# Kernel tuning notes

Measured on AMD Instinct MI355X. Metric: run time of the kernel, lower is better.

The kernel has to match this reference:

```python
import jax, jax.numpy as jnp
import numpy as np

G, K1, K2, N, NP, EPS = 16, 128, 32, 128, 512, 1e-5

def _bn(x, axes):
    m = jnp.mean(x, axes, keepdims=True)
    v = jnp.var(x, axes, keepdims=True)  # biased, as torch BN training mode
    return (x - m) * jax.lax.rsqrt(v + EPS)

def _fps(xyz, npoint):
    # farthest point sampling, deterministic start at index 0; xyz (B,P,3)
    B, P, _ = xyz.shape
    def step(carry, _):
        dists, far = carry
        c = jnp.take_along_axis(xyz, far[:, None, None], axis=1)   # (B,1,3)
        d = jnp.sum((xyz - c) ** 2, -1)                            # (B,P)
        dists = jnp.minimum(dists, d)
        return (dists, jnp.argmax(dists, -1)), far
    init = (jnp.full((B, P), 1e10, xyz.dtype), jnp.zeros((B,), jnp.int32))
    _, idx = jax.lax.scan(step, init, None, length=npoint)         # (npoint,B)
    return jnp.take_along_axis(xyz, idx.T[:, :, None], axis=1)     # (B,npoint,3)

def _pointnet(x, w1, b1, w2, b2, w3, b3):
    h = jax.nn.relu(_bn(x @ w1 + b1, (0, 1)))
    h = jax.nn.relu(_bn(h @ w2 + b2, (0, 1)))
    h = _bn(h @ w3 + b3, (0, 1))
    return jnp.max(h, axis=1)                                      # (B,1024)

def _mapping(feat, w1, b1, w2, b2, w3, b3, w4, b4):
    # all 16 branches stacked on leading axis g
    h = jax.nn.relu(_bn(jnp.einsum('bk,gkj->gbj', feat, w1) + b1[:, None, :], (1,)))
    h = jax.nn.relu(_bn(jnp.einsum('gbj,gjk->gbk', h, w2) + b2[:, None, :], (1,)))
    h = jax.nn.relu(_bn(jnp.einsum('gbj,gjk->gbk', h, w3) + b3[:, None, :], (1,)))
    return jax.nn.relu(_bn(jnp.einsum('gbj,gjk->gbk', h, w4) + b4[:, None, :], (1,)))

def _axform(feat, fw, fb, c1w, c1b, c2w, c2b, c3w, c3b, c4w, c4b):
    # feat (G,B,K1); 1x1 convs expressed as einsums in channels-last layout
    xb = (jnp.einsum('gbk,gkm->gbm', feat, fw) + fb[:, None, :]).reshape(G, -1, N, K2)
    h = jax.nn.relu(_bn(jnp.einsum('gbnk,gkc->gbnc', xb, c1w) + c1b[:, None, None, :], (1, 2)))
    h = jax.nn.relu(_bn(jnp.einsum('gbnc,gcd->gbnd', h, c2w) + c2b[:, None, None, :], (1, 2)))
    h = jnp.einsum('gbnd,gde->gbne', h, c3w) + c3b[:, None, None, :]  # (G,B,N,1024)
    w = jax.nn.softmax(h, axis=2)                                     # softmax over N
    y = jnp.einsum('gbne,gbnk->gbek', w, xb)                          # (G,B,1024,K2)
    return jnp.einsum('gbek,gkc->gbec', y, c4w) + c4b[:, None, None, :]  # (G,B,1024,3)

def _forward(x, pn, mp, gen, ref):
    x_partial = _fps(x, NP)                                           # (B,512,3)
    feat = _pointnet(x, *pn)                                          # (B,1024)
    mfeat = _mapping(feat, *mp)                                       # (G,B,K1)
    x1g = _axform(mfeat, *gen)                                        # (G,B,1024,3)
    B = x.shape[0]
    x_1 = jnp.transpose(x1g, (1, 0, 2, 3)).reshape(B, -1, 3)          # (B,16384,3)
    fps1 = jax.vmap(lambda p: _fps(p, NP))(x1g)                       # (G,B,512,3)
    x_base = jnp.concatenate([fps1, jnp.broadcast_to(x_partial, (G,) + x_partial.shape)], axis=2)
    x2g = x_base + _axform(mfeat, *ref)                               # (G,B,1024,3)
    x_2 = jnp.transpose(x2g, (1, 0, 2, 3)).reshape(B, -1, 3)
    return x_1, x_2

def setup_inputs() -> dict:
    keys = iter(jax.random.split(jax.random.key(0), 40))
    def rn(shape, s=0.02):
        return (s * jax.random.normal(next(keys), shape)).astype(jnp.float32)
    inp = {}
    inp['x'] = jax.random.normal(next(keys), (16, 2048, 3), jnp.float32)
    inp['pn_w1'] = rn((3, 64));      inp['pn_b1'] = rn((64,))
    inp['pn_w2'] = rn((64, 128));    inp['pn_b2'] = rn((128,))
    inp['pn_w3'] = rn((128, 1024));  inp['pn_b3'] = rn((1024,))
    inp['mp_w1'] = rn((G, 1024, 1024)); inp['mp_b1'] = rn((G, 1024))
    inp['mp_w2'] = rn((G, 1024, 1024)); inp['mp_b2'] = rn((G, 1024))
    inp['mp_w3'] = rn((G, 1024, 1024)); inp['mp_b3'] = rn((G, 1024))
    inp['mp_w4'] = rn((G, 1024, K1));   inp['mp_b4'] = rn((G, K1))
    for p in ('g', 'r'):
        inp[p + '_fw'] = rn((G, K1, N * K2)); inp[p + '_fb'] = rn((G, N * K2))
        inp[p + '_c1w'] = rn((G, K2, 64));    inp[p + '_c1b'] = rn((G, 64))
        inp[p + '_c2w'] = rn((G, 64, 128));   inp[p + '_c2b'] = rn((G, 128))
        inp[p + '_c3w'] = rn((G, 128, 1024)); inp[p + '_c3b'] = rn((G, 1024))
        inp[p + '_c4w'] = rn((G, K2, 3));     inp[p + '_c4b'] = rn((G, 3))
    return inp

def reference(x, pn_w1, pn_b1, pn_w2, pn_b2, pn_w3, pn_b3,
              mp_w1, mp_b1, mp_w2, mp_b2, mp_w3, mp_b3, mp_w4, mp_b4,
              g_fw, g_fb, g_c1w, g_c1b, g_c2w, g_c2b, g_c3w, g_c3b, g_c4w, g_c4b,
              r_fw, r_fb, r_c1w, r_c1b, r_c2w, r_c2b, r_c3w, r_c3b, r_c4w, r_c4b):
    pn = (pn_w1, pn_b1, pn_w2, pn_b2, pn_w3, pn_b3)
    mp = (mp_w1, mp_b1, mp_w2, mp_b2, mp_w3, mp_b3, mp_w4, mp_b4)
    gen = (g_fw, g_fb, g_c1w, g_c1b, g_c2w, g_c2b, g_c3w, g_c3b, g_c4w, g_c4b)
    ref = (r_fw, r_fb, r_c1w, r_c1b, r_c2w, r_c2b, r_c3w, r_c3b, r_c4w, r_c4b)
    return _forward(x, pn, mp, gen, ref)
```

## Files before the change

### kernel.cpp

```cpp
#include <hip/hip_runtime.h>
#include <math.h>

#define TID ((int)threadIdx.x)

namespace {
constexpr float EPSf = 1e-5f;

typedef __attribute__((ext_vector_type(8))) short short8;
typedef __attribute__((ext_vector_type(4))) float f32x4;

struct FpsArgs {
  const float* pts; float* out; float* dmin; int* far;
  int it0, it1, nc;
};

__device__ __forceinline__ unsigned fenc(float f){
  unsigned u = __float_as_uint(f);
  return (u & 0x80000000u) ? ~u : (u | 0x80000000u);
}
__device__ __forceinline__ float fdec(unsigned e){
  unsigned u = (e & 0x80000000u) ? (e & 0x7fffffffu) : ~e;
  return __uint_as_float(u);
}
__device__ __forceinline__ short bf16rne(float f){
  unsigned u = __float_as_uint(f);
  return (short)((u + 0x7fffu + ((u >> 16) & 1u)) >> 16);
}

template<int CTRL>
__device__ __forceinline__ void dpp_comb(float& bm, int& bp){
  int om_i = __builtin_amdgcn_update_dpp(__float_as_int(bm), __float_as_int(bm), CTRL, 0xf, 0xf, false);
  int op   = __builtin_amdgcn_update_dpp(bp, bp, CTRL, 0xf, 0xf, false);
  float om = __int_as_float(om_i);
  if (om > bm || (om == bm && op < bp)){ bm = om; bp = op; }
}

template<int LP, int NT>
__device__ void fps_body(const FpsArgs& a, int ci){
  const int NPTS = NT*LP;
  const float* pts = a.pts + (size_t)ci * NPTS * 3;
  float* out = a.out + (size_t)ci * 512 * 3;
  float* dst = a.dmin + (size_t)ci * NPTS;
  float px[LP], py[LP], pz[LP], dmin[LP];
#pragma unroll
  for (int j = 0; j < LP; j++){
    int p = TID + NT*j;
    px[j] = pts[p*3+0]; py[j] = pts[p*3+1]; pz[j] = pts[p*3+2];
  }
  int far;
  if (a.it0 == 0){
#pragma unroll
    for (int j = 0; j < LP; j++) dmin[j] = 1e10f;
    far = 0;
  } else {
#pragma unroll
    for (int j = 0; j < LP; j++) dmin[j] = dst[TID + NT*j];
    far = a.far[ci];
  }
  __shared__ unsigned long long red2[2][NT/64];
  for (int i = a.it0; i < a.it1; i++){
    float cx = pts[far*3+0], cy = pts[far*3+1], cz = pts[far*3+2];
    if (TID == 0){ out[i*3+0]=cx; out[i*3+1]=cy; out[i*3+2]=cz; }
    float bm = -1.f; int bp = 0;
#pragma unroll
    for (int j = 0; j < LP; j++){
      float dx = __fsub_rn(px[j], cx);
      float dy = __fsub_rn(py[j], cy);
      float dz = __fsub_rn(pz[j], cz);
      float d  = __fadd_rn(__fadd_rn(__fmul_rn(dx,dx), __fmul_rn(dy,dy)), __fmul_rn(dz,dz));
      float dm = fminf(dmin[j], d);
      dmin[j] = dm;
      if (dm > bm){ bm = dm; bp = TID + NT*j; }
    }
    dpp_comb<0x111>(bm,bp); dpp_comb<0x112>(bm,bp); dpp_comb<0x114>(bm,bp);
    dpp_comb<0x118>(bm,bp); dpp_comb<0x142>(bm,bp); dpp_comb<0x143>(bm,bp);
    unsigned long long key =
      ((unsigned long long)(unsigned)__builtin_amdgcn_readlane(__float_as_int(bm), 63) << 32)
      | (unsigned)~(unsigned)__builtin_amdgcn_readlane(bp, 63);
    if ((TID & 63) == 63) red2[i&1][TID>>6] = key;
    __syncthreads();
    unsigned long long kk = red2[i&1][0];
#pragma unroll
    for (int t = 1; t < NT/64; t++){
      unsigned long long o = red2[i&1][t];
      kk = kk > o ? kk : o;
    }
    far = (int)~(unsigned)kk;
  }
  if (a.it1 < 512){
#pragma unroll
    for (int j = 0; j < LP; j++) dst[TID + NT*j] = dmin[j];
    if (TID == 0) a.far[ci] = far;
  }
}

template<int C, int K, int FLP>
__global__ void __launch_bounds__(256) rowgemm_kernel(const float* __restrict__ in,
    const float* __restrict__ w, const float* __restrict__ bias, const float2* __restrict__ st2,
    float* __restrict__ out, int rows_per_g, FpsArgs fa)
{
  int bid = blockIdx.x;
  if constexpr (FLP > 0){
    if (bid < fa.nc){ fps_body<FLP,256>(fa, bid); return; }
    bid -= fa.nc;
  }
  constexpr int RPB = 256 / C;
  __shared__ float lin[RPB * K];
  size_t row0 = (size_t)bid * RPB;
  int g = (int)(row0 / rows_per_g);
  for (int i = TID; i < RPB*K; i += 256){
    float v = in[row0*(size_t)K + i];
    if (st2){ float2 s = st2[(size_t)g*K + (i % K)]; v = fmaxf((v - s.x)*s.y, 0.f); }
    lin[i] = v;
  }
  __syncthreads();
  int r = TID / C, c = TID % C;
  float acc = bias[(size_t)g*C + c];
  const float* wg = w + (size_t)g*K*C + c;
#pragma unroll
  for (int k = 0; k < K; k++) acc = fmaf(lin[r*K + k], wg[(size_t)k*C], acc);
  out[(row0 + r)*C + c] = acc;
}

template<int FLP>
__global__ void __launch_bounds__(256, 4) big1024m_kernel(const float* __restrict__ in,
    const float2* __restrict__ st2, const short* __restrict__ wtp,
    float* __restrict__ ps, float* __restrict__ pq, unsigned* __restrict__ maxenc, FpsArgs fa)
{
  int bid = blockIdx.x;
  if constexpr (FLP > 0){
    if (bid < fa.nc){ fps_body<FLP,256>(fa, bid); return; }
    bid -= fa.nc;
  }
  size_t row0 = (size_t)bid * 128;
  int b = (int)(row0 >> 11);
  __shared__ float2 sb[128];
  __shared__ float mS[512], mQ[512], mM[512];
  if (TID < 128) sb[TID] = st2[TID];
  __syncthreads();
  int lane = TID & 63, wid = TID >> 6, lr = lane & 15, lkg = lane >> 4;

  short8 afr[4][2];
  const float* src = in + row0*128;
#pragma unroll
  for (int kt = 0; kt < 4; kt++){
    int kb = kt*32 + lkg*8;
    float2 ss[8];
#pragma unroll
    for (int j = 0; j < 8; j++) ss[j] = sb[kb + j];
#pragma unroll
    for (int nt = 0; nt < 2; nt++){
      int row = wid*32 + nt*16 + lr;
      float4 a0 = *(const float4*)(src + row*128 + kb);
      float4 a1 = *(const float4*)(src + row*128 + kb + 4);
      const float vals[8] = {a0.x,a0.y,a0.z,a0.w,a1.x,a1.y,a1.z,a1.w};
      short8 ob;
#pragma unroll
      for (int j = 0; j < 8; j++)
        ob[j] = bf16rne(fmaxf((vals[j] - ss[j].x)*ss[j].y, 0.f));
      afr[kt][nt] = ob;
    }
  }

  for (int cs = 0; cs < 8; cs++){
    f32x4 acc[2][8];
#pragma unroll
    for (int nt = 0; nt < 2; nt++)
#pragma unroll
      for (int et = 0; et < 8; et++) acc[nt][et] = (f32x4){0.f,0.f,0.f,0.f};
    const short* wp = wtp + (size_t)(cs*128)*128;
#pragma unroll
    for (int kt = 0; kt < 4; kt++){
      int kb = kt*32 + lkg*8;
#pragma unroll
      for (int et = 0; et < 8; et++){
        short8 bfr = *(const short8*)&wp[(et*16 + lr)*128 + kb];
        acc[0][et] = __builtin_amdgcn_mfma_f32_16x16x32_bf16(afr[kt][0], bfr, acc[0][et], 0, 0, 0);
        acc[1][et] = __builtin_amdgcn_mfma_f32_16x16x32_bf16(afr[kt][1], bfr, acc[1][et], 0, 0, 0);
      }
    }
#pragma unroll
    for (int et = 0; et < 8; et++){
      float s = 0.f, q = 0.f, m = -1e38f;
#pragma unroll
      for (int nt = 0; nt < 2; nt++)
#pragma unroll
        for (int r = 0; r < 4; r++){
          float v = acc[nt][et][r];
          s += v; q = fmaf(v, v, q); m = fmaxf(m, v);
        }
      s += __shfl_xor(s, 16); s += __shfl_xor(s, 32);
      q += __shfl_xor(q, 16); q += __shfl_xor(q, 32);
      m = fmaxf(m, __shfl_xor(m, 16)); m = fmaxf(m, __shfl_xor(m, 32));
      if (lkg == 0){
        mS[wid*128 + et*16 + lr] = s;
        mQ[wid*128 + et*16 + lr] = q;
        mM[wid*128 + et*16 + lr] = m;
      }
    }
    __syncthreads();
    if (wid == 0){
#pragma unroll
      for (int t = 0; t < 2; t++){
        int c = t*64 + lane;
        float s4 = mS[c] + mS[128 + c] + mS[256 + c] + mS[384 + c];
        float q4 = mQ[c] + mQ[128 + c] + mQ[256 + c] + mQ[384 + c];
        float m4 = fmaxf(fmaxf(mM[c], mM[128 + c]), fmaxf(mM[256 + c], mM[384 + c]));
        ps[(size_t)bid*1024 + cs*128 + c] = s4;
        pq[(size_t)bid*1024 + cs*128 + c] = q4;
        atomicMax(&maxenc[(size_t)b*1024 + cs*128 + c], fenc(m4));
      }
    }
    __syncthreads();
  }
}

template<int FLP>
__global__ void __launch_bounds__(128) mapgemm2_kernel(const float* __restrict__ in, int in_gstride,
    const float* __restrict__ w, const float* __restrict__ bias, const float2* __restrict__ st2,
    float* __restrict__ out, int K, int J, int JB, int NS, FpsArgs fa)
{
  int bid = blockIdx.x;
  if constexpr (FLP > 0){
    if (bid < fa.nc){ fps_body<FLP,128>(fa, bid); return; }
    bid -= fa.nc;
  }
  int kc = bid / (JB*16);
  int g  = (bid / JB) % 16;
  int jb = bid % JB;
  int kchunk = K / NS, k0 = kc*kchunk;
  __shared__ float linT[128*16];
  const float* ing = in + (size_t)g * in_gstride;
  for (int i = TID; i < kchunk*16; i += 128){
    int b = i / kchunk, k = i - b*kchunk;
    float v = ing[(size_t)b*K + k0 + k];
    if (st2){ float2 s = st2[(size_t)g*K + k0 + k]; v = fmaxf((v - s.x)*s.y, 0.f); }
    linT[k*16 + b] = v;
  }
  __syncthreads();
  int bh = TID >> 6, jq = TID & 63;
  int j = jb*256 + jq*4;
  const float* wp = w + ((size_t)g*K + k0)*J + j;
  float4 a4[8];
#pragma unroll
  for (int bi = 0; bi < 8; bi++) a4[bi] = make_float4(0.f,0.f,0.f,0.f);
#pragma unroll 4
  for (int k = 0; k < kchunk; k++){
    float4 wv = *(const float4*)(wp + (size_t)k*J);
    float4 l0 = *(const float4*)&linT[k*16 + bh*8];
    float4 l1 = *(const float4*)&linT[k*16 + bh*8 + 4];
    const float lv[8] = {l0.x,l0.y,l0.z,l0.w,l1.x,l1.y,l1.z,l1.w};
#pragma unroll
    for (int bi = 0; bi < 8; bi++){
      a4[bi].x = fmaf(lv[bi], wv.x, a4[bi].x);
      a4[bi].y = fmaf(lv[bi], wv.y, a4[bi].y);
      a4[bi].z = fmaf(lv[bi], wv.z, a4[bi].z);
      a4[bi].w = fmaf(lv[bi], wv.w, a4[bi].w);
    }
  }
  if (NS == 1){
    float4 bv = *(const float4*)(bias + (size_t)g*J + j);
#pragma unroll
    for (int bi = 0; bi < 8; bi++){
      int b = bh*8 + bi;
      float4 o = make_float4(a4[bi].x+bv.x, a4[bi].y+bv.y, a4[bi].z+bv.z, a4[bi].w+bv.w);
      *(float4*)&out[((size_t)g*16 + b)*J + j] = o;
    }
  } else {
#pragma unroll
    for (int bi = 0; bi < 8; bi++)
      *(float4*)&out[(((size_t)kc*16 + g)*16 + bh*8 + bi)*J + j] = a4[bi];
  }
}

__global__ void __launch_bounds__(256) mapgemm_kernel(const float* __restrict__ in, int in_gstride,
    const float* __restrict__ w, const float* __restrict__ bias, const float2* __restrict__ st2,
    float* __restrict__ out, int K, int J, int JB, int NS)
{
  int bid = blockIdx.x;
  int kc = bid / (JB*16);
  int g  = (bid / JB) % 16;
  int jb = bid % JB;
  int j  = jb*256 + TID;
  bool jv = j < J;
  int jc = jv ? j : 0;
  int kchunk = K / NS;
  int k0 = kc * kchunk;
  __shared__ float lin[16 * 128];
  const float* ing = in + (size_t)g * in_gstride;
  float acc[16];
  float bv = (NS == 1 && jv) ? bias[(size_t)g*J + jc] : 0.f;
#pragma unroll
  for (int b = 0; b < 16; b++) acc[b] = bv;
  for (int kt = k0; kt < k0 + kchunk; kt += 128){
    __syncthreads();
    for (int i = TID; i < 2048; i += 256){
      int b = i >> 7, k = i & 127;
      float v = ing[(size_t)b*K + kt + k];
      if (st2){ float2 s = st2[(size_t)g*K + kt + k]; v = fmaxf((v - s.x)*s.y, 0.f); }
      lin[i] = v;
    }
    __syncthreads();
    const float* wg = w + ((size_t)g*K + kt)*J + jc;
    for (int k = 0; k < 128; k++){
      float wv = wg[(size_t)k*J];
#pragma unroll
      for (int b = 0; b < 16; b++) acc[b] = fmaf(lin[b*128 + k], wv, acc[b]);
    }
  }
  if (jv){
    if (NS == 1){
      for (int b = 0; b < 16; b++) out[((size_t)g*16 + b)*J + j] = acc[b];
    } else {
      for (int b = 0; b < 16; b++) out[(((size_t)kc*16 + g)*16 + b)*J + j] = acc[b];
    }
  }
}

__global__ void __launch_bounds__(256) redstats_kernel(const float* __restrict__ part,
    const float* __restrict__ bias, float* __restrict__ out, float2* __restrict__ st2,
    int J, int NS)
{
  int t = blockIdx.x*256 + TID;
  int g = t / J, j = t % J;
  float bv = bias[t];
  float s = 0.f, q = 0.f;
  for (int b = 0; b < 16; b++){
    float v = bv;
    for (int c = 0; c < NS; c++) v += part[(((size_t)c*16 + g)*16 + b)*J + j];
    out[((size_t)g*16 + b)*J + j] = v;
    s += v; q = fmaf(v, v, q);
  }
  float mean = s * (1.f/16.f);
  float var  = q * (1.f/16.f) - mean*mean;
  st2[t] = make_float2(mean, rsqrtf(fmaxf(var, 0.f) + EPSf));
}

template<int FLP>
__global__ void __launch_bounds__(256) statsacc_kernel(const float* __restrict__ in,
    float* __restrict__ part, int C, size_t chunk, FpsArgs fa)
{
  int bid = blockIdx.x;
  if constexpr (FLP > 0){
    if (bid < fa.nc){ fps_body<FLP,256>(fa, bid); return; }
    bid -= fa.nc;
  }
  size_t base = (size_t)bid * chunk;
  int c = TID % C;
  float s = 0.f, q = 0.f;
  for (size_t idx = base + TID; idx < base + chunk; idx += 256){
    float v = in[idx]; s += v; q = fmaf(v, v, q);
  }
  __shared__ float ls[256], lq[256];
  ls[TID] = s; lq[TID] = q; __syncthreads();
  if (TID < C){
    for (int t = TID + C; t < 256; t += C){ s += ls[t]; q += lq[t]; }
    part[((size_t)bid*C + c)*2]   = s;
    part[((size_t)bid*C + c)*2+1] = q;
  }
}

__global__ void statsfin_kernel(const float* __restrict__ part, float2* __restrict__ st2,
    int C, int G, float invR)
{
  int slot = blockIdx.x*256 + TID;
  if (slot >= G*C) return;
  int g = slot / C, c = slot % C;
  int bpg = 256 / G;
  float s = 0.f, q = 0.f;
  for (int b = 0; b < bpg; b++){
    size_t p = ((size_t)(g*bpg + b)*C + c)*2;
    s += part[p]; q += part[p+1];
  }
  float mean = s*invR;
  float var  = q*invR - mean*mean;
  st2[slot] = make_float2(mean, rsqrtf(fmaxf(var, 0.f) + EPSf));
}

__global__ void pnfin_kernel(const float* __restrict__ ps, const float* __restrict__ pq,
                             float2* __restrict__ st)
{
  int c = blockIdx.x*256 + TID;
  float s = 0.f, q = 0.f;
  for (int rb = 0; rb < 256; rb++){ s += ps[rb*1024 + c]; q += pq[rb*1024 + c]; }
  float mean = s * (1.f/32768.f);
  float var  = q * (1.f/32768.f) - mean*mean;
  st[c] = make_float2(mean, rsqrtf(fmaxf(var, 0.f) + EPSf));
}

__global__ void feat_kernel(const unsigned* __restrict__ me, const float2* __restrict__ st,
                            float* __restrict__ feat)
{
  int t = blockIdx.x*256 + TID;
  int c = t & 1023;
  float2 s = st[c];
  feat[t] = (fdec(me[t]) - s.x) * s.y;
}

__global__ void __launch_bounds__(256) wtr_kernel(const float* __restrict__ c3w,
                                                  short* __restrict__ wt)
{
  int g = blockIdx.x >> 4, kt = blockIdx.x & 15;
  __shared__ float lds[8*1024];
  const float* src = c3w + ((size_t)g*128 + kt*8)*1024;
  for (int i = TID; i < 8192; i += 256) lds[i] = src[i];
  __syncthreads();
  for (int e = TID; e < 1024; e += 256){
    short8 v;
#pragma unroll
    for (int j = 0; j < 8; j++) v[j] = bf16rne(lds[j*1024 + e]);
    *(short8*)&wt[((size_t)g*1024 + e)*128 + kt*8] = v;
  }
}

template<int FLP>
__global__ void __launch_bounds__(256, 2) fused_kernel(const float* __restrict__ c2o,
    const float2* __restrict__ st2, const short* __restrict__ wt,
    const float* __restrict__ xb, const float* __restrict__ c4w, const float* __restrict__ c4b,
    float* __restrict__ out_pts, float* __restrict__ out_x1, FpsArgs fa)
{
  int bid = blockIdx.x;
  if constexpr (FLP > 0){
    if (bid < fa.nc){ fps_body<FLP,256>(fa, bid); return; }
    bid -= fa.nc;
  }
  int gb = bid >> 1, ebh = bid & 1;
  int g = gb >> 4, b = gb & 15;
  __shared__ short Pbf[16384];
  __shared__ short Bls[16384];
  __shared__ short xbT[4096];
  __shared__ float2 sb[128];
  __shared__ float mred[512];

  if (TID < 128) sb[TID] = st2[(size_t)g*128 + TID];
  {
    const float* xsrc = xb + (size_t)gb*4096;
    for (int idx = TID; idx < 1024; idx += 256){
      int n = idx >> 3, k4 = (idx & 7)*4;
      float4 v = *(const float4*)(xsrc + n*32 + k4);
      const float vv[4] = {v.x, v.y, v.z, v.w};
#pragma unroll
      for (int j = 0; j < 4; j++){
        int k = k4 + j;
        xbT[k*128 + (((n >> 3) ^ (k & 7)) << 3) + (n & 7)] = bf16rne(vv[j]);
      }
    }
  }
  const int eb0 = ebh*4;
  const short* wt_base = wt + (size_t)g*1024*128;
  {
    const short* wtg = wt_base + (size_t)(eb0*128)*128;
    for (int i = TID; i < 2048; i += 256){
      int e = i >> 4, kc = i & 15;
      short8 v = *(const short8*)&wtg[e*128 + kc*8];
      *(short8*)&Bls[e*128 + ((kc ^ (e & 7)) << 3)] = v;
    }
  }

  int lane = TID & 63, wid = TID >> 6;
  int lr = lane & 15, lkg = lane >> 4;

  __syncthreads();

  short8 afr[4][2];
  const float* src = c2o + (size_t)gb*16384;
#pragma unroll
  for (int kt = 0; kt < 4; kt++){
    int kb = kt*32 + lkg*8;
    float2 ss[8];
#pragma unroll
    for (int j = 0; j < 8; j++) ss[j] = sb[kb + j];
#pragma unroll
    for (int nt = 0; nt < 2; nt++){
      int row = wid*32 + nt*16 + lr;
      float4 a0 = *(const float4*)(src + row*128 + kb);
      float4 a1 = *(const float4*)(src + row*128 + kb + 4);
      const float vals[8] = {a0.x,a0.y,a0.z,a0.w,a1.x,a1.y,a1.z,a1.w};
      short8 ob;
#pragma unroll
      for (int j = 0; j < 8; j++)
        ob[j] = bf16rne(fmaxf((vals[j] - ss[j].x)*ss[j].y, 0.f));
      afr[kt][nt] = ob;
    }
  }

  float c4l[2][3];
  {
    const float* cw = c4w + g*96;
#pragma unroll
    for (int kt2 = 0; kt2 < 2; kt2++){
      int k = kt2*16 + lr;
      c4l[kt2][0] = cw[k*3+0]; c4l[kt2][1] = cw[k*3+1]; c4l[kt2][2] = cw[k*3+2];
    }
  }
  float cb0 = c4b[g*3+0], cb1 = c4b[g*3+1], cb2 = c4b[g*3+2];
  unsigned* Pu = (unsigned*)Pbf;

  for (int eb = eb0; eb < eb0 + 4; eb++){
    f32x4 acc[2][8];
#pragma unroll
    for (int nt = 0; nt < 2; nt++)
#pragma unroll
      for (int et = 0; et < 8; et++) acc[nt][et] = (f32x4){0.f,0.f,0.f,0.f};
#pragma unroll
    for (int kt = 0; kt < 4; kt++){
      int kcf = kt*4 + lkg;
#pragma unroll
      for (int et = 0; et < 8; et++){
        int e = et*16 + lr;
        short8 bfr = *(const short8*)&Bls[e*128 + ((kcf ^ (e & 7)) << 3)];
        acc[0][et] = __builtin_amdgcn_mfma_f32_16x16x32_bf16(afr[kt][0], bfr, acc[0][et], 0, 0, 0);
        acc[1][et] = __builtin_amdgcn_mfma_f32_16x16x32_bf16(afr[kt][1], bfr, acc[1][et], 0, 0, 0);
      }
    }

    short8 bpre[8];
    bool havepre = (eb + 1 < eb0 + 4);
    if (havepre){
      const short* wtg = wt_base + (size_t)((eb+1)*128)*128;
#pragma unroll
      for (int ii = 0; ii < 8; ii++){
        int i = TID + 256*ii;
        int e = i >> 4, kc = i & 15;
        bpre[ii] = *(const short8*)&wtg[e*128 + kc*8];
      }
    }

#pragma unroll
    for (int et = 0; et < 8; et++){
      float ss = 0.f;
#pragma unroll
      for (int nt = 0; nt < 2; nt++)
#pragma unroll
        for (int r = 0; r < 4; r++){
          float p = __expf(acc[nt][et][r]);
          acc[nt][et][r] = p;
          ss += p;
        }
      ss += __shfl_xor(ss, 16);
      ss += __shfl_xor(ss, 32);
      if (lkg == 0) mred[wid*128 + et*16 + lr] = ss;
      int e = et*16 + lr;
#pragma unroll
      for (int nt = 0; nt < 2; nt++){
        int nb = wid*32 + nt*16 + lkg*4;
        int base = e*128 + ((((nb >> 3)) ^ (e & 7)) << 3) + (nb & 7);
        unsigned lo = (unsigned)(unsigned short)bf16rne(acc[nt][et][0])
                    | ((unsigned)(unsigned short)bf16rne(acc[nt][et][1]) << 16);
        unsigned hi = (unsigned)(unsigned short)bf16rne(acc[nt][et][2])
                    | ((unsigned)(unsigned short)bf16rne(acc[nt][et][3]) << 16);
        Pu[base >> 1]       = lo;
        Pu[(base >> 1) + 1] = hi;
      }
    }
    __syncthreads();

    if (havepre){
#pragma unroll
      for (int ii = 0; ii < 8; ii++){
        int i = TID + 256*ii;
        int e = i >> 4, kc = i & 15;
        *(short8*)&Bls[e*128 + ((kc ^ (e & 7)) << 3)] = bpre[ii];
      }
    }

    f32x4 yy[2][2];
#pragma unroll
    for (int t2 = 0; t2 < 2; t2++){ yy[t2][0] = (f32x4){0.f,0.f,0.f,0.f}; yy[t2][1] = (f32x4){0.f,0.f,0.f,0.f}; }
#pragma unroll
    for (int nc = 0; nc < 4; nc++){
      short8 bfrs[2];
#pragma unroll
      for (int kt2 = 0; kt2 < 2; kt2++){
        int k = kt2*16 + lr;
        bfrs[kt2] = *(const short8*)&xbT[k*128 + (((nc*4 + lkg) ^ (k & 7)) << 3)];
      }
#pragma unroll
      for (int t2 = 0; t2 < 2; t2++){
        int e = (wid*2 + t2)*16 + lr;
        short8 afrp = *(const short8*)&Pbf[e*128 + (((nc*4 + lkg) ^ (e & 7)) << 3)];
        yy[t2][0] = __builtin_amdgcn_mfma_f32_16x16x32_bf16(afrp, bfrs[0], yy[t2][0], 0, 0, 0);
        yy[t2][1] = __builtin_amdgcn_mfma_f32_16x16x32_bf16(afrp, bfrs[1], yy[t2][1], 0, 0, 0);
      }
    }

#pragma unroll
    for (int t2 = 0; t2 < 2; t2++){
#pragma unroll
      for (int r = 0; r < 4; r++){
        float o0 = yy[t2][0][r]*c4l[0][0] + yy[t2][1][r]*c4l[1][0];
        float o1 = yy[t2][0][r]*c4l[0][1] + yy[t2][1][r]*c4l[1][1];
        float o2 = yy[t2][0][r]*c4l[0][2] + yy[t2][1][r]*c4l[1][2];
#pragma unroll
        for (int d = 1; d < 16; d <<= 1){
          o0 += __shfl_xor(o0, d);
          o1 += __shfl_xor(o1, d);
          o2 += __shfl_xor(o2, d);
        }
        if (lr == 0){
          int e = (wid*2 + t2)*16 + lkg*4 + r;
          float s = mred[e] + mred[128 + e] + mred[256 + e] + mred[384 + e];
          float rs = 1.f / s;
          o0 = fmaf(o0, rs, cb0);
          o1 = fmaf(o1, rs, cb1);
          o2 = fmaf(o2, rs, cb2);
          int eg = eb*128 + e;
          size_t po = ((size_t)gb*1024 + eg)*3;
          out_pts[po+0] = o0; out_pts[po+1] = o1; out_pts[po+2] = o2;
          if (out_x1){
            size_t xo = (((size_t)b*16 + g)*1024 + eg)*3;
            out_x1[xo+0] = o0; out_x1[xo+1] = o1; out_x1[xo+2] = o2;
          }
        }
      }
    }
    __syncthreads();
  }
}

__global__ void combine_kernel(const float* __restrict__ fps1, const float* __restrict__ xpart,
                               const float* __restrict__ d2, float* __restrict__ x2)
{
  size_t i = (size_t)blockIdx.x*256 + TID;
  if (i >= (size_t)16*16*1024*3) return;
  int c = (int)(i % 3);
  size_t t = i / 3;
  int e = (int)(t % 1024);
  size_t gb = t / 1024;
  int g = (int)(gb >> 4), b = (int)(gb & 15);
  float base;
  if (e < 512) base = fps1[(gb*512 + e)*3 + c];
  else         base = xpart[((size_t)b*512 + (e - 512))*3 + c];
  x2[(((size_t)b*16384) + (size_t)g*1024 + e)*3 + c] = base + d2[i];
}

}

extern "C" void kernel_launch(void* const* d_in, const int* in_sizes, int n_in,
                              void* d_out, int out_size, void* d_ws, size_t ws_size,
                              hipStream_t stream)
{
  (void)in_sizes; (void)n_in; (void)out_size; (void)ws_size;
  const float* x    = (const float*)d_in[0];
  const float* pnw1 = (const float*)d_in[1];
  const float* pnb1 = (const float*)d_in[2];
  const float* pnw2 = (const float*)d_in[3];
  const float* pnb2 = (const float*)d_in[4];
  const float* pnw3 = (const float*)d_in[5];
  const float* mpw[4] = {(const float*)d_in[7],(const float*)d_in[9],(const float*)d_in[11],(const float*)d_in[13]};
  const float* mpb[4] = {(const float*)d_in[8],(const float*)d_in[10],(const float*)d_in[12],(const float*)d_in[14]};

  float* ws = (float*)d_ws;
  size_t o = 0;
  auto alloc = [&](size_t n){ float* p = ws + o; o += n; return p; };
  float* x_partial = alloc(24576);
  float* feat      = alloc(16384);
  float* mfeat     = alloc(32768);
  float2* st_pn1   = (float2*)alloc(128);
  float2* st_pn2   = (float2*)alloc(256);
  float2* st_pn3   = (float2*)alloc(2048);
  float2* st_c1    = (float2*)alloc(2048);
  float2* st_c2    = (float2*)alloc(4096);
  float2* st_map0  = (float2*)alloc(32768);
  float2* st_map1  = (float2*)alloc(32768);
  float2* st_map2  = (float2*)alloc(32768);
  float2* st_map3  = (float2*)alloc(4096);
  float* sa_part   = alloc(65536);
  float* pn_ps     = alloc(262144);
  float* pn_pq     = alloc(262144);
  unsigned* maxenc = (unsigned*)alloc(16384);
  float* mapA      = alloc(262144);
  float* mapB      = alloc(262144);
  float* mpart     = alloc(4194304);
  float* xb        = alloc(1048576);
  float* c1o       = alloc(2097152);
  float* c2o       = alloc(4194304);
  float* x1g       = alloc(786432);
  float* d2buf     = alloc(786432);
  float* fps1b     = alloc(393216);
  float* fpsA_dmin = alloc(32768);
  int*   fpsA_far  = (int*)alloc(16);
  float* fpsB_dmin = alloc(262144);
  int*   fpsB_far  = (int*)alloc(256);
  short* wt_g      = (short*)alloc(1048576);
  short* wt_r      = (short*)alloc(1048576);
  short* wt_pn     = (short*)alloc(65536);

  float* xout1 = (float*)d_out;
  float* xout2 = xout1 + 786432;

  hipMemsetAsync(maxenc, 0, 16384*sizeof(unsigned), stream);

  wtr_kernel<<<256, 256, 0, stream>>>((const float*)d_in[21], wt_g);
  wtr_kernel<<<256, 256, 0, stream>>>((const float*)d_in[31], wt_r);
  wtr_kernel<<<16, 256, 0, stream>>>(pnw3, wt_pn);

  FpsArgs f0{};
  FpsArgs fa{x, x_partial, fpsA_dmin, fpsA_far, 0, 0, 16};

  fa.it0 = 0; fa.it1 = 64;
  rowgemm_kernel<64,3,8><<<8192+16, 256, 0, stream>>>(x, pnw1, pnb1, nullptr, c1o, 32768, fa);
  statsacc_kernel<0><<<256, 256, 0, stream>>>(c1o, sa_part, 64, 8192, f0);
  statsfin_kernel<<<1, 256, 0, stream>>>(sa_part, st_pn1, 64, 1, 1.f/32768.f);
  fa.it0 = 64; fa.it1 = 128;
  rowgemm_kernel<128,64,8><<<16384+16, 256, 0, stream>>>(c1o, pnw2, pnb2, st_pn1, c2o, 32768, fa);
  statsacc_kernel<0><<<256, 256, 0, stream>>>(c2o, sa_part, 128, 16384, f0);
  statsfin_kernel<<<1, 256, 0, stream>>>(sa_part, st_pn2, 128, 1, 1.f/32768.f);
  fa.it0 = 128; fa.it1 = 224;
  big1024m_kernel<8><<<256+16, 256, 0, stream>>>(c2o, st_pn2, wt_pn, pn_ps, pn_pq, maxenc, fa);
  pnfin_kernel<<<4, 256, 0, stream>>>(pn_ps, pn_pq, st_pn3);
  feat_kernel<<<64, 256, 0, stream>>>(maxenc, st_pn3, feat);

  fa.it0 = 224; fa.it1 = 288;
  mapgemm2_kernel<16><<<1024+16, 128, 0, stream>>>(feat, 0,     mpw[0], nullptr, nullptr, mpart, 1024, 1024, 4, 16, fa);
  redstats_kernel<<<64, 256, 0, stream>>>(mpart, mpb[0], mapA, st_map0, 1024, 16);
  fa.it0 = 288; fa.it1 = 352;
  mapgemm2_kernel<16><<<1024+16, 128, 0, stream>>>(mapA, 16384, mpw[1], nullptr, st_map0, mpart, 1024, 1024, 4, 16, fa);
  redstats_kernel<<<64, 256, 0, stream>>>(mpart, mpb[1], mapB, st_map1, 1024, 16);
  fa.it0 = 352; fa.it1 = 416;
  mapgemm2_kernel<16><<<1024+16, 128, 0, stream>>>(mapB, 16384, mpw[2], nullptr, st_map1, mpart, 1024, 1024, 4, 16, fa);
  redstats_kernel<<<64, 256, 0, stream>>>(mpart, mpb[2], mapA, st_map2, 1024, 16);
  mapgemm_kernel<<<64, 256, 0, stream>>>(mapA, 16384, mpw[3], nullptr, st_map2, mpart, 1024, 128, 1, 4);
  redstats_kernel<<<8, 256, 0, stream>>>(mpart, mpb[3], mfeat, st_map3, 128, 4);

  for (int p = 0; p < 2; p++){
    const float* fw  = (const float*)d_in[15 + p*10 + 0];
    const float* fb  = (const float*)d_in[15 + p*10 + 1];
    const float* c1w = (const float*)d_in[15 + p*10 + 2];
    const float* c1b = (const float*)d_in[15 + p*10 + 3];
    const float* c2w = (const float*)d_in[15 + p*10 + 4];
    const float* c2b = (const float*)d_in[15 + p*10 + 5];
    const float* c4w = (const float*)d_in[15 + p*10 + 8];
    const float* c4b = (const float*)d_in[15 + p*10 + 9];

    if (p == 0){
      fa.it0 = 416; fa.it1 = 480;
      mapgemm2_kernel<16><<<256+16, 128, 0, stream>>>(mfeat, 2048, fw, fb, st_map3, xb, 128, 4096, 16, 1, fa);
      fa.it0 = 480; fa.it1 = 512;
      rowgemm_kernel<64,32,8><<<8192+16, 256, 0, stream>>>(xb, c1w, c1b, nullptr, c1o, 2048, fa);
      statsacc_kernel<0><<<256, 256, 0, stream>>>(c1o, sa_part, 64, 8192, f0);
      statsfin_kernel<<<4, 256, 0, stream>>>(sa_part, st_c1, 64, 16, 1.f/2048.f);
      rowgemm_kernel<128,64,0><<<16384, 256, 0, stream>>>(c1o, c2w, c2b, st_c1, c2o, 2048, f0);
      statsacc_kernel<0><<<256, 256, 0, stream>>>(c2o, sa_part, 128, 16384, f0);
      statsfin_kernel<<<8, 256, 0, stream>>>(sa_part, st_c2, 128, 16, 1.f/2048.f);
      fused_kernel<0><<<512, 256, 0, stream>>>(c2o, st_c2, wt_g, xb, c4w, c4b, x1g, xout1, f0);
    } else {
      FpsArgs fb_{x1g, fps1b, fpsB_dmin, fpsB_far, 0, 0, 256};
      fb_.it0 = 0; fb_.it1 = 48;
      mapgemm2_kernel<8><<<256+256, 128, 0, stream>>>(mfeat, 2048, fw, fb, st_map3, xb, 128, 4096, 16, 1, fb_);
      fb_.it0 = 48; fb_.it1 = 144;
      rowgemm_kernel<64,32,4><<<8192+256, 256, 0, stream>>>(xb, c1w, c1b, nullptr, c1o, 2048, fb_);
      fb_.it0 = 144; fb_.it1 = 176;
      statsacc_kernel<4><<<256+256, 256, 0, stream>>>(c1o, sa_part, 64, 8192, fb_);
      statsfin_kernel<<<4, 256, 0, stream>>>(sa_part, st_c1, 64, 16, 1.f/2048.f);
      fb_.it0 = 176; fb_.it1 = 288;
      rowgemm_kernel<128,64,4><<<16384+256, 256, 0, stream>>>(c1o, c2w, c2b, st_c1, c2o, 2048, fb_);
      fb_.it0 = 288; fb_.it1 = 320;
      statsacc_kernel<4><<<256+256, 256, 0, stream>>>(c2o, sa_part, 128, 16384, fb_);
      statsfin_kernel<<<8, 256, 0, stream>>>(sa_part, st_c2, 128, 16, 1.f/2048.f);
      fb_.it0 = 320; fb_.it1 = 512;
      fused_kernel<4><<<512+256, 256, 0, stream>>>(c2o, st_c2, wt_r, xb, c4w, c4b, d2buf, nullptr, fb_);
    }
  }

  combine_kernel<<<3072, 256, 0, stream>>>(fps1b, x_partial, d2buf, xout2);
}
```

Measured before the change: 1.622 ms.

## Replace scalar 64->128 conv GEMMs with bf16 MFMA kernel using pre-transposed weights

Adds a c2m kernel that computes the 64->128 layer (pointnet layer 2 and the c2 convs of both branches) with bf16 16x16x32 MFMA on 128-row tiles. It applies the previous BN and ReLU while converting activations to bf16, and reads weights pre-converted by a new wtr2 kernel into an XOR-swizzled LDS layout. This replaces the scalar FMA rowgemm, which launched one block per two rows, and cuts the block count from 16384 to 256. The FPS iteration ranges co-scheduled with these kernels are rebalanced to match. In exchange it adds bf16 rounding to these layers' inputs and weights, plus three small weight-transpose launches.

```diff
diff --git a/kernel.cpp b/kernel.cpp
--- a/kernel.cpp
+++ b/kernel.cpp
@@ -120,6 +120,83 @@
 #pragma unroll
   for (int k = 0; k < K; k++) acc = fmaf(lin[r*K + k], wg[(size_t)k*C], acc);
   out[(row0 + r)*C + c] = acc;
+}
+
+template<int FLP>
+__global__ void __launch_bounds__(256, 4) c2m_kernel(const float* __restrict__ in,
+    const float2* __restrict__ st1, const short* __restrict__ wt,
+    const float* __restrict__ bias, float* __restrict__ out, int rows_per_g, FpsArgs fa)
+{
+  int bid = blockIdx.x;
+  if constexpr (FLP > 0){
+    if (bid < fa.nc){ fps_body<FLP,256>(fa, bid); return; }
+    bid -= fa.nc;
+  }
+  size_t row0 = (size_t)bid * 128;
+  int g = (int)(row0 / rows_per_g);
+  __shared__ short Bls[8192];
+  __shared__ float2 sb[64];
+  if (TID < 64) sb[TID] = st1[(size_t)g*64 + TID];
+  {
+    const short* wg = wt + (size_t)g*8192;
+    for (int i = TID; i < 1024; i += 256){
+      int c = i >> 3, kc = i & 7;
+      short8 v = *(const short8*)&wg[c*64 + kc*8];
+      *(short8*)&Bls[c*64 + ((kc ^ (c & 7)) << 3)] = v;
+    }
+  }
+  __syncthreads();
+  int lane = TID & 63, wid = TID >> 6, lr = lane & 15, lkg = lane >> 4;
+
+  short8 afr[2][2];
+  const float* src = in + row0*64;
+#pragma unroll
+  for (int kt = 0; kt < 2; kt++){
+    int kb = kt*32 + lkg*8;
+    float2 ss[8];
+#pragma unroll
+    for (int j = 0; j < 8; j++) ss[j] = sb[kb + j];
+#pragma unroll
+    for (int nt = 0; nt < 2; nt++){
+      int row = wid*32 + nt*16 + lr;
+      float4 a0 = *(const float4*)(src + row*64 + kb);
+      float4 a1 = *(const float4*)(src + row*64 + kb + 4);
+      const float vals[8] = {a0.x,a0.y,a0.z,a0.w,a1.x,a1.y,a1.z,a1.w};
+      short8 ob;
+#pragma unroll
+      for (int j = 0; j < 8; j++)
+        ob[j] = bf16rne(fmaxf((vals[j] - ss[j].x)*ss[j].y, 0.f));
+      afr[kt][nt] = ob;
+    }
+  }
+
+  f32x4 acc[2][8];
+#pragma unroll
+  for (int nt = 0; nt < 2; nt++)
+#pragma unroll
+    for (int et = 0; et < 8; et++) acc[nt][et] = (f32x4){0.f,0.f,0.f,0.f};
+#pragma unroll
+  for (int kt = 0; kt < 2; kt++){
+#pragma unroll
+    for (int et = 0; et < 8; et++){
+      int e = et*16 + lr;
+      short8 bfr = *(const short8*)&Bls[e*64 + (((kt*4 + lkg) ^ (e & 7)) << 3)];
+      acc[0][et] = __builtin_amdgcn_mfma_f32_16x16x32_bf16(afr[kt][0], bfr, acc[0][et], 0, 0, 0);
+      acc[1][et] = __builtin_amdgcn_mfma_f32_16x16x32_bf16(afr[kt][1], bfr, acc[1][et], 0, 0, 0);
+    }
+  }
+
+#pragma unroll
+  for (int et = 0; et < 8; et++){
+    float bv = bias[(size_t)g*128 + et*16 + lr];
+#pragma unroll
+    for (int nt = 0; nt < 2; nt++)
+#pragma unroll
+      for (int r = 0; r < 4; r++){
+        int row = wid*32 + nt*16 + lkg*4 + r;
+        out[(row0 + row)*128 + et*16 + lr] = acc[nt][et][r] + bv;
+      }
+  }
 }
 
 template<int FLP>
@@ -410,6 +487,23 @@
 #pragma unroll
     for (int j = 0; j < 8; j++) v[j] = bf16rne(lds[j*1024 + e]);
     *(short8*)&wt[((size_t)g*1024 + e)*128 + kt*8] = v;
+  }
+}
+
+__global__ void __launch_bounds__(256) wtr2_kernel(const float* __restrict__ w,
+                                                   short* __restrict__ wt)
+{
+  int g = blockIdx.x;
+  __shared__ float lds[8192];
+  const float* src = w + (size_t)g*8192;
+  for (int i = TID; i < 8192; i += 256) lds[i] = src[i];
+  __syncthreads();
+  for (int i = TID; i < 1024; i += 256){
+    int c = i >> 3, kc = i & 7;
+    short8 v;
+#pragma unroll
+    for (int j = 0; j < 8; j++) v[j] = bf16rne(lds[(kc*8 + j)*128 + c]);
+    *(short8*)&wt[(size_t)g*8192 + c*64 + kc*8] = v;
   }
 }
 
@@ -644,7 +738,6 @@
   const float* x    = (const float*)d_in[0];
   const float* pnw1 = (const float*)d_in[1];
   const float* pnb1 = (const float*)d_in[2];
-  const float* pnw2 = (const float*)d_in[3];
   const float* pnb2 = (const float*)d_in[4];
   const float* pnw3 = (const float*)d_in[5];
   const float* mpw[4] = {(const float*)d_in[7],(const float*)d_in[9],(const float*)d_in[11],(const float*)d_in[13]};
@@ -685,6 +778,9 @@
   short* wt_g      = (short*)alloc(1048576);
   short* wt_r      = (short*)alloc(1048576);
   short* wt_pn     = (short*)alloc(65536);
+  short* wt_pn2    = (short*)alloc(4096);
+  short* wt_c2g    = (short*)alloc(65536);
+  short* wt_c2r    = (short*)alloc(65536);
 
   float* xout1 = (float*)d_out;
   float* xout2 = xout1 + 786432;
@@ -694,6 +790,9 @@
   wtr_kernel<<<256, 256, 0, stream>>>((const float*)d_in[21], wt_g);
   wtr_kernel<<<256, 256, 0, stream>>>((const float*)d_in[31], wt_r);
   wtr_kernel<<<16, 256, 0, stream>>>(pnw3, wt_pn);
+  wtr2_kernel<<<1, 256, 0, stream>>>((const float*)d_in[3],  wt_pn2);
+  wtr2_kernel<<<16, 256, 0, stream>>>((const float*)d_in[19], wt_c2g);
+  wtr2_kernel<<<16, 256, 0, stream>>>((const float*)d_in[29], wt_c2r);
 
   FpsArgs f0{};
   FpsArgs fa{x, x_partial, fpsA_dmin, fpsA_far, 0, 0, 16};
@@ -703,7 +802,7 @@
   statsacc_kernel<0><<<256, 256, 0, stream>>>(c1o, sa_part, 64, 8192, f0);
   statsfin_kernel<<<1, 256, 0, stream>>>(sa_part, st_pn1, 64, 1, 1.f/32768.f);
   fa.it0 = 64; fa.it1 = 128;
-  rowgemm_kernel<128,64,8><<<16384+16, 256, 0, stream>>>(c1o, pnw2, pnb2, st_pn1, c2o, 32768, fa);
+  c2m_kernel<8><<<256+16, 256, 0, stream>>>(c1o, st_pn1, wt_pn2, pnb2, c2o, 32768, fa);
   statsacc_kernel<0><<<256, 256, 0, stream>>>(c2o, sa_part, 128, 16384, f0);
   statsfin_kernel<<<1, 256, 0, stream>>>(sa_part, st_pn2, 128, 1, 1.f/32768.f);
   fa.it0 = 128; fa.it1 = 224;
@@ -728,10 +827,10 @@
     const float* fb  = (const float*)d_in[15 + p*10 + 1];
     const float* c1w = (const float*)d_in[15 + p*10 + 2];
     const float* c1b = (const float*)d_in[15 + p*10 + 3];
-    const float* c2w = (const float*)d_in[15 + p*10 + 4];
     const float* c2b = (const float*)d_in[15 + p*10 + 5];
     const float* c4w = (const float*)d_in[15 + p*10 + 8];
     const float* c4b = (const float*)d_in[15 + p*10 + 9];
+    const short* wtc2 = (p == 0) ? wt_c2g : wt_c2r;
 
     if (p == 0){
       fa.it0 = 416; fa.it1 = 480;
@@ -740,7 +839,7 @@
       rowgemm_kernel<64,32,8><<<8192+16, 256, 0, stream>>>(xb, c1w, c1b, nullptr, c1o, 2048, fa);
       statsacc_kernel<0><<<256, 256, 0, stream>>>(c1o, sa_part, 64, 8192, f0);
       statsfin_kernel<<<4, 256, 0, stream>>>(sa_part, st_c1, 64, 16, 1.f/2048.f);
-      rowgemm_kernel<128,64,0><<<16384, 256, 0, stream>>>(c1o, c2w, c2b, st_c1, c2o, 2048, f0);
+      c2m_kernel<0><<<256, 256, 0, stream>>>(c1o, st_c1, wtc2, c2b, c2o, 2048, f0);
       statsacc_kernel<0><<<256, 256, 0, stream>>>(c2o, sa_part, 128, 16384, f0);
       statsfin_kernel<<<8, 256, 0, stream>>>(sa_part, st_c2, 128, 16, 1.f/2048.f);
       fused_kernel<0><<<512, 256, 0, stream>>>(c2o, st_c2, wt_g, xb, c4w, c4b, x1g, xout1, f0);
@@ -753,12 +852,12 @@
       fb_.it0 = 144; fb_.it1 = 176;
       statsacc_kernel<4><<<256+256, 256, 0, stream>>>(c1o, sa_part, 64, 8192, fb_);
       statsfin_kernel<<<4, 256, 0, stream>>>(sa_part, st_c1, 64, 16, 1.f/2048.f);
-      fb_.it0 = 176; fb_.it1 = 288;
-      rowgemm_kernel<128,64,4><<<16384+256, 256, 0, stream>>>(c1o, c2w, c2b, st_c1, c2o, 2048, fb_);
-      fb_.it0 = 288; fb_.it1 = 320;
+      fb_.it0 = 176; fb_.it1 = 240;
+      c2m_kernel<4><<<256+256, 256, 0, stream>>>(c1o, st_c1, wtc2, c2b, c2o, 2048, fb_);
+      fb_.it0 = 240; fb_.it1 = 272;
       statsacc_kernel<4><<<256+256, 256, 0, stream>>>(c2o, sa_part, 128, 16384, fb_);
       statsfin_kernel<<<8, 256, 0, stream>>>(sa_part, st_c2, 128, 16, 1.f/2048.f);
-      fb_.it0 = 320; fb_.it1 = 512;
+      fb_.it0 = 272; fb_.it1 = 512;
       fused_kernel<4><<<512+256, 256, 0, stream>>>(c2o, st_c2, wt_r, xb, c4w, c4b, d2buf, nullptr, fb_);
     }
   }
```

Measured after the change: 1.595 ms (median of 2 runs). Within noise of the previous version (-1.7%).
